# Optimization experiments

Hardware: AMD Instinct MI355X
Metric: run time of the kernel (lower is better)

## Reference

```python
import math
import jax, jax.numpy as jnp
import numpy as np

H = 256      # d_model (number of SSM copies)
N = 32       # half state size (conjugate symmetry)
R = 1        # low-rank correction rank
CH = 1       # channels
L_MAX = 8192 # kernel length (l_max, rate=1.0)


def _r2c(x):
    return x[..., 0] + 1j * x[..., 1]


def _conj(x):
    return jnp.concatenate([x, jnp.conj(x)], axis=-1)


def _mat_power(A, L):
    # A: (H, M, M), L python int; binary exponentiation (powers of A commute)
    out = jnp.broadcast_to(jnp.eye(A.shape[-1], dtype=A.dtype), A.shape)
    while L > 0:
        if L & 1:
            out = jnp.einsum('hij,hjk->hik', out, A)
        A = jnp.einsum('hij,hjk->hik', A, A)
        L >>= 1
    return out


def setup_inputs():
    key = jax.random.key(0)
    ks = jax.random.split(key, 6)
    # log_dt in [log(1e-3), log(1e-1)] as in S4 init
    log_dt = math.log(1e-3) + jax.random.uniform(ks[0], (H,)) * (math.log(1e-1) - math.log(1e-3))
    # inv_w_real = log(-w_real); w_real in (-1.5, -0.5) -> stable discrete system
    inv_w_real = jnp.log(0.5 + jax.random.uniform(ks[1], (H, N)))
    # HiPPO-like imaginary parts: pi * n per state, small jitter
    w_imag = math.pi * jnp.broadcast_to(jnp.arange(N, dtype=jnp.float32), (H, N)) \
             + 0.01 * jax.random.normal(ks[2], (H, N))
    P = 0.5 * jax.random.normal(ks[3], (R, H, N, 2))   # real view of complex (R,H,N)
    B = jax.random.normal(ks[4], (1, H, N, 2))          # real view of complex (1,H,N)
    C = jax.random.normal(ks[5], (CH, H, N, 2))         # real view of complex (CH,H,N)
    return {
        'log_dt': log_dt.astype(jnp.float32),
        'inv_w_real': inv_w_real.astype(jnp.float32),
        'w_imag': w_imag.astype(jnp.float32),
        'P': P.astype(jnp.float32),
        'B': B.astype(jnp.float32),
        'C': C.astype(jnp.float32),
    }


def _kernel(log_dt, inv_w_real, w_imag, P, B, C):
    dt = jnp.exp(log_dt)                              # (H,)  rate = 1.0
    w = -jnp.exp(inv_w_real) + 1j * w_imag            # (H, N) real_type='exp'
    Pc = _r2c(P)                                      # (R, H, N)
    Bc = _r2c(B)                                      # (1, H, N)
    Cc = _r2c(C)                                      # (CH, H, N)
    Qc = jnp.conj(Pc)                                 # (R, H, N)

    # ---- _setup_linear: bilinear-transform discretization pieces ----
    D = 1.0 / (2.0 / dt[:, None] - w)                 # (H, N)
    E = 2.0 / dt[:, None] + w                         # (H, N)
    Rm = jnp.eye(R, dtype=jnp.float32) + 2.0 * jnp.real(
        jnp.einsum('rhn,hn,shn->hrs', Qc, D, Pc))     # (H, R, R)
    QD = jnp.einsum('rhn,hn->hrn', Qc, D)             # (H, R, N)
    Rs = jnp.linalg.solve(Rm.astype(QD.dtype), QD)    # (H, R, N)
    Rs = jnp.transpose(Rs, (1, 0, 2))                 # (R, H, N)

    # ---- _setup_state: dA acting on full 2N-dim (conjugated) state ----
    Dc, Ec, Pc2, Qc2, Rc = (_conj(x) for x in (D, E, Pc, Qc, Rs))
    M = 2 * N
    state = jnp.broadcast_to(jnp.eye(M, dtype=jnp.complex64)[:, None, :], (M, H, M))
    ns = Ec * state - jnp.einsum('rhn,rhm,bhm->bhn', Pc2, Qc2, state)
    ns = Dc * (ns - jnp.einsum('rhn,rhm,bhm->bhn', Pc2, Rc, ns))
    dA = jnp.transpose(ns, (1, 2, 0))                 # (H, M, M)

    # ---- _setup_C: C~ = (I - dA^L)^T C (truncated back to N) ----
    dA_L = _mat_power(dA, L_MAX)                      # (H, M, M)
    C_ = _conj(Cc)                                    # (CH, H, M)
    prod = jnp.einsum('hnm,chn->chm', dA_L, C_)       # contract with dA_L^T
    C_t = (C_ - prod)[..., :N]                        # (CH, H, N)

    # ---- forward: FFT nodes, Cauchy matvec, Woodbury, irfft ----
    Lf = L_MAX // 2 + 1
    omega = jnp.asarray(np.exp(-2j * np.pi / L_MAX), dtype=jnp.complex64) ** jnp.arange(Lf)
    z = 2 * (1 - omega) / (1 + omega)                 # (Lf,)
    w_dt = w * dt[:, None]                            # (H, N)

    Bcat = jnp.concatenate([Bc, Pc], axis=0)          # (1+R, H, N)
    Ccat = jnp.concatenate([C_t, Qc], axis=0)         # (CH+R, H, N)
    v = Bcat[:, None] * Ccat[None]                    # (1+R, CH+R, H, N)
    v = v * dt[None, None, :, None]

    # cauchy_naive with conjugate-pair symmetry
    v_full = _conj(v)                                 # (1+R, CH+R, H, 2N)
    w_full = _conj(w_dt)                              # (H, 2N)
    cauchy = 1.0 / (z[None, None, :] - w_full[..., None])  # (H, 2N, Lf)
    r = jnp.einsum('abhn,hnl->abhl', v_full, cauchy)  # (1+R, CH+R, H, Lf)

    # rank-1 Woodbury correction
    k_f = r[:-1, :-1] - r[:-1, -1:] * r[-1:, :-1] / (1 + r[-1:, -1:])
    k_f = k_f * 2 / (1 + omega)
    k = jnp.fft.irfft(k_f, n=L_MAX, axis=-1)          # (1, CH, H, L)
    return k[-1]                                      # (CH, H, L)


def reference(log_dt, inv_w_real, w_imag, P, B, C):
    return _kernel(log_dt, inv_w_real, w_imag, P, B, C)
```

## Files before the change

### kernel.cpp

```cpp
#include <hip/hip_runtime.h>


#define HH 256
#define NN 32
#define MF 4096

typedef float2 c32;

__device__ __forceinline__ c32 cmul(c32 a, c32 b){ return make_float2(a.x*b.x - a.y*b.y, a.x*b.y + a.y*b.x); }
__device__ __forceinline__ c32 cadd(c32 a, c32 b){ return make_float2(a.x+b.x, a.y+b.y); }
__device__ __forceinline__ c32 csub(c32 a, c32 b){ return make_float2(a.x-b.x, a.y-b.y); }
__device__ __forceinline__ c32 cconjf(c32 a){ return make_float2(a.x, -a.y); }
__device__ __forceinline__ float frcp(float x){ return __builtin_amdgcn_rcpf(x); }

__device__ __forceinline__ float dpp_xor1(float x){
  return __int_as_float(__builtin_amdgcn_update_dpp(0, __float_as_int(x), 0xB1, 0xF, 0xF, true));
}
__device__ __forceinline__ float dpp_xor2(float x){
  return __int_as_float(__builtin_amdgcn_update_dpp(0, __float_as_int(x), 0x4E, 0xF, 0xF, true));
}

__global__ __launch_bounds__(512, 2)
void ssk_S(const float* __restrict__ log_dt, const float* __restrict__ invwr,
           const float* __restrict__ wim, const float* __restrict__ Pin,
           const float* __restrict__ Cin, float* __restrict__ Sws)
{
  __shared__ __align__(16) float4 tA[36];
  __shared__ c32 tB[36];
  __shared__ float red[8*64];
  const int bid = blockIdx.x;
  const int h = bid >> 1;
  const int base = (bid & 1) << 11;
  const int tid = threadIdx.x;

  if (tid < 64) {
    const int n = tid & 31;
    const bool cj = tid >= 32;
    const float dt = expf(log_dt[h]);
    float wr = -expf(invwr[h*NN + n]);
    float wi = wim[h*NN + n];
    if (cj) wi = -wi;
    const float tdt = 2.0f / dt;
    float dr = tdt - wr, di = -wi;
    float invd = 1.0f / (dr*dr + di*di);
    c32 D = make_float2(dr*invd, -di*invd);
    c32 E = make_float2(tdt + wr, wi);
    c32 Pf = make_float2(Pin[(h*NN+n)*2], Pin[(h*NN+n)*2+1]);
    if (cj) Pf.y = -Pf.y;
    c32 Cf = make_float2(Cin[(h*NN+n)*2], Cin[(h*NN+n)*2+1]);
    if (cj) Cf.y = -Cf.y;
    float rm = (Pf.x*Pf.x + Pf.y*Pf.y) * D.x;
    #pragma unroll
    for (int off = 32; off >= 1; off >>= 1) rm += __shfl_xor(rm, off, 64);
    rm += 1.0f;
    c32 Rc = cmul(cconjf(Pf), D);
    float invrm = 1.0f / rm;
    Rc.x *= invrm; Rc.y *= invrm;
    c32 RP = cmul(Rc, Pf);
    #pragma unroll
    for (int off = 32; off >= 1; off >>= 1) {
      RP.x += __shfl_xor(RP.x, off, 64);
      RP.y += __shfl_xor(RP.y, off, 64);
    }
    c32 Q2 = cconjf(Pf);
    c32 s  = csub(cmul(Rc, E), cmul(RP, Q2));
    c32 u  = cadd(Q2, s);
    c32 dd = cmul(D, E);
    c32 pp = cmul(D, Pf);
    c32 pc = cmul(pp, Cf);
    c32 pu = cmul(pp, u);
    if (tid < 32) {
      const int pm = tid + (tid >> 3);
      float ba = 2.0f*(pc.x*dd.x + pc.y*dd.y);
      float bb = 2.0f*(pu.x*dd.x + pu.y*dd.y);
      tA[pm] = make_float4(dd.x, dd.y, pc.x + pc.x, ba);
      tB[pm] = make_float2(pu.x + pu.x, bb);
    }
  }
  __syncthreads();

  const int sub = tid & 3;
  const int grp = tid >> 2;
  const int pbase = sub * 9;

  float pdx[8], pdy[8], paa[8], pba[8], pab[8], pbb[8];
  #pragma unroll
  for (int k = 0; k < 8; k++) {
    float4 A = tA[pbase + k];
    c32 Bv = tB[pbase + k];
    pdx[k] = A.x; pdy[k] = A.y; paa[k] = A.z; pba[k] = A.w;
    pab[k] = Bv.x; pbb[k] = Bv.y;
  }

  float U1x[8], U2x[8];
  #pragma unroll
  for (int k = 0; k < 8; k++) { U1x[k] = 0.0f; U2x[k] = 0.0f; }

  for (int it = 0; it < 16; it++) {
    const int j = base + (it << 7) + grp;
    float rev = (float)j * (1.0f/8192.0f);
    float zx = __builtin_amdgcn_cosf(rev);
    float zy = __builtin_amdgcn_sinf(rev);
    float t2zy = zy + zy;

    float iwxA[8], iwyA[8];
    float Px = 0.0f, Py = 0.0f, Qx = 0.0f, Qy = 0.0f;
    float Rx = 0.0f, Ry = 0.0f, Sx = 0.0f, Sy = 0.0f;
    #pragma unroll
    for (int k = 0; k < 8; k++) {
      float dxx = zx - pdx[k];
      float dy1 = zy - pdy[k];
      float dy2 = zy + pdy[k];
      float xx  = dxx*dxx;
      float p12 = dy1*dy2;
      float wvx = xx - p12;
      float wvyn = dxx*t2zy;
      float den = fmaf(wvx, wvx, wvyn*wvyn);
      float ip  = frcp(den);
      float iwx = wvx*ip;
      float iwy = -wvyn*ip;
      iwxA[k] = iwx; iwyA[k] = iwy;
      Px = fmaf(paa[k], iwx, Px); Py = fmaf(paa[k], iwy, Py);
      Qx = fmaf(pba[k], iwx, Qx); Qy = fmaf(pba[k], iwy, Qy);
      Rx = fmaf(pab[k], iwx, Rx); Ry = fmaf(pab[k], iwy, Ry);
      Sx = fmaf(pbb[k], iwx, Sx); Sy = fmaf(pbb[k], iwy, Sy);
    }
    float ax = fmaf(zx, Px, fmaf(-zy, Py, -Qx));
    float ay = fmaf(zx, Py, fmaf( zy, Px, -Qy));
    float bx = fmaf(zx, Rx, fmaf(-zy, Ry, -Sx));
    float by = fmaf(zx, Ry, fmaf( zy, Rx, -Sy));
    ax += dpp_xor1(ax); ax += dpp_xor2(ax);
    ay += dpp_xor1(ay); ay += dpp_xor2(ay);
    bx += dpp_xor1(bx); bx += dpp_xor2(bx);
    by += dpp_xor1(by); by += dpp_xor2(by);
    float denq = 1.0f + bx, deny = by;
    float idn = frcp(fmaf(denq, denq, deny*deny));
    float tx = (ax*denq + ay*deny)*idn;
    float ty = (ay*denq - ax*deny)*idn;
    float qx = zx*tx - zy*ty;
    float qy = zx*ty + zy*tx;
    if (j == 0) { qx *= 0.5f; qy *= 0.5f; }
    float qzx = qx*zx - qy*zy;
    float qzy = fmaf(qx, zy, qy*zx);
    #pragma unroll
    for (int k = 0; k < 8; k++) {
      float iwx = iwxA[k], iwy = iwyA[k];
      U1x[k] = fmaf(qx,  iwx, fmaf(-qy,  iwy, U1x[k]));
      U2x[k] = fmaf(qzx, iwx, fmaf(-qzy, iwy, U2x[k]));
    }
  }

  float ssx[8], ssy[8];
  #pragma unroll
  for (int k = 0; k < 8; k++) {
    ssx[k] = fmaf(-(pdx[k] + pdx[k]), U1x[k], U2x[k] + U2x[k]);
    ssy[k] = (pdy[k] + pdy[k]) * U1x[k];
  }

  #pragma unroll
  for (int off = 4; off <= 32; off <<= 1) {
    #pragma unroll
    for (int k = 0; k < 8; k++) {
      ssx[k] += __shfl_xor(ssx[k], off, 64);
      ssy[k] += __shfl_xor(ssy[k], off, 64);
    }
  }
  const int lane = tid & 63;
  const int wv = tid >> 6;
  if (lane < 4) {
    #pragma unroll
    for (int k = 0; k < 8; k++) {
      red[wv*64 + lane*16 + 2*k]     = ssx[k];
      red[wv*64 + lane*16 + 2*k + 1] = ssy[k];
    }
  }
  __syncthreads();

  if (tid < 64) {
    float t = 0.0f;
    #pragma unroll
    for (int w = 0; w < 8; w++) t += red[w*64 + tid];
    Sws[bid*64 + tid] = t;
  }
}

__global__ __launch_bounds__(1024, 4)
void ssk_B(const float* __restrict__ log_dt, const float* __restrict__ invwr,
           const float* __restrict__ wim, const float* __restrict__ Pin,
           const float* __restrict__ Bin, const float* __restrict__ Cin,
           const float* __restrict__ Sws, c32* __restrict__ out)
{
  __shared__ __align__(16) c32 Xs[4098];
  __shared__ __align__(16) c32 Zs[4096];
  __shared__ __align__(16) float4 cs1_s[NN];
  __shared__ __align__(16) float4 cs2_s[NN];
  __shared__ c32 cs3_s[NN];
  const int h = blockIdx.x;
  const int tid = threadIdx.x;

  if (tid < 64) {
    const int n = tid & 31;
    const bool cj = tid >= 32;
    const float dt = expf(log_dt[h]);
    float wr = -expf(invwr[h*NN + n]);
    float wi = wim[h*NN + n];
    if (cj) wi = -wi;
    const float tdt = 2.0f / dt;
    float dr = tdt - wr, di = -wi;
    float invd = 1.0f / (dr*dr + di*di);
    c32 D = make_float2(dr*invd, -di*invd);
    c32 E = make_float2(tdt + wr, wi);
    c32 Pf = make_float2(Pin[(h*NN+n)*2], Pin[(h*NN+n)*2+1]);
    if (cj) Pf.y = -Pf.y;
    c32 Cf = make_float2(Cin[(h*NN+n)*2], Cin[(h*NN+n)*2+1]);
    if (cj) Cf.y = -Cf.y;
    float rm = (Pf.x*Pf.x + Pf.y*Pf.y) * D.x;
    #pragma unroll
    for (int off = 32; off >= 1; off >>= 1) rm += __shfl_xor(rm, off, 64);
    rm += 1.0f;
    c32 Rc = cmul(cconjf(Pf), D);
    float invrm = 1.0f / rm;
    Rc.x *= invrm; Rc.y *= invrm;
    c32 RP = cmul(Rc, Pf);
    #pragma unroll
    for (int off = 32; off >= 1; off >>= 1) {
      RP.x += __shfl_xor(RP.x, off, 64);
      RP.y += __shfl_xor(RP.y, off, 64);
    }
    c32 Q2 = cconjf(Pf);
    c32 s  = csub(cmul(Rc, E), cmul(RP, Q2));
    c32 u  = cadd(Q2, s);
    c32 dd = cmul(D, E);
    c32 pp = cmul(D, Pf);
    c32 pc = cmul(pp, Cf);
    c32 pu = cmul(pp, u);

    float dxxn = -1.0f - dd.x;
    float nn1 = fmaf(dxxn, dxxn, dd.y*dd.y);
    float ii = frcp(nn1);
    float glxn = dxxn*ii, glyn = dd.y*ii;
    float aterm = 2.0f*(pc.x*glxn - pc.y*glyn);
    float bterm = 2.0f*(pu.x*glxn - pu.y*glyn);
    #pragma unroll
    for (int off = 16; off >= 1; off >>= 1) {
      aterm += __shfl_xor(aterm, off, 64);
      bterm += __shfl_xor(bterm, off, 64);
    }

    if (tid < 32) {
      const int m = tid;
      c32 dL = dd;
      #pragma unroll
      for (int i2 = 0; i2 < 13; i2++) dL = cmul(dL, dL);
      c32 S;
      S.x = Sws[h*128 + 2*m]     + Sws[h*128 + 64 + 2*m];
      S.y = Sws[h*128 + 2*m + 1] + Sws[h*128 + 64 + 2*m + 1];
      float qn = -aterm * frcp(1.0f + bterm) * 0.5f;
      S.x += qn * 2.0f * glxn;
      S.y += qn * 2.0f * glyn;
      c32 y = cmul(Cf, dL);
      c32 uS = cmul(u, S);
      y.x -= uS.x * (1.0f/8192.0f);
      y.y -= uS.y * (1.0f/8192.0f);
      c32 Ct = csub(Cf, y);
      c32 Bc = make_float2(Bin[(h*NN+m)*2], Bin[(h*NN+m)*2+1]);
      c32 Qc = cconjf(Pf);
      c32 v00 = cmul(Bc, Ct), v01 = cmul(Bc, Qc), v10 = cmul(Pf, Ct), v11 = cmul(Pf, Qc);
      float wx = wr*dt, wy = wi*dt;
      float aw = fmaf(wx, wx, wy*wy);
      float tnw = -(wx + wx);
      float td = dt + dt;
      float a00 = td*v00.x, b00 = td*(v00.x*wx + v00.y*wy);
      float a01 = td*v01.x, b01 = td*(v01.x*wx + v01.y*wy);
      float a10 = td*v10.x, b10 = td*(v10.x*wx + v10.y*wy);
      float a11 = td*v11.x, b11 = td*(v11.x*wx + v11.y*wy);
      cs1_s[m] = make_float4(aw, tnw, a00, b00);
      cs2_s[m] = make_float4(a01, b01, a10, b10);
      cs3_s[m] = make_float2(a11, b11);
      float s00 = v00.x * dt;
      #pragma unroll
      for (int off = 16; off >= 1; off >>= 1) s00 += __shfl_xor(s00, off, 64);
      if (m == 0) Xs[MF] = make_float2(s00, 0.0f);
    }
  }
  __syncthreads();

  {
    float Tq[4], t2[4], t2sq[4];
    c32 a00[4], a01[4], a10[4], a11[4];
    #pragma unroll
    for (int q = 0; q < 4; q++) {
      int j = tid + (q << 10);
      float rev = (float)j * (1.0f/16384.0f);
      float sn = __builtin_amdgcn_sinf(rev);
      float cs = __builtin_amdgcn_cosf(rev);
      float T = sn * frcp(cs);
      Tq[q] = T; t2[q] = 2.0f*T; t2sq[q] = t2[q]*t2[q];
      a00[q] = make_float2(0,0); a01[q] = make_float2(0,0);
      a10[q] = make_float2(0,0); a11[q] = make_float2(0,0);
    }
    #pragma unroll 2
    for (int n = 0; n < NN; n++) {
      float4 C1 = cs1_s[n];
      float4 C2 = cs2_s[n];
      c32   C3 = cs3_s[n];
      #pragma unroll
      for (int q = 0; q < 4; q++) {
        float wvx = C1.x - t2sq[q];
        float wvy = C1.y * t2[q];
        float r = frcp(fmaf(wvx, wvx, wvy*wvy));
        float iwx = wvx*r;
        float iwy = -wvy*r;
        float at;
        at = C1.z*t2[q];
        a00[q].x = fmaf(-C1.w, iwx, fmaf(-at, iwy, a00[q].x));
        a00[q].y = fmaf(-C1.w, iwy, fmaf( at, iwx, a00[q].y));
        at = C2.x*t2[q];
        a01[q].x = fmaf(-C2.y, iwx, fmaf(-at, iwy, a01[q].x));
        a01[q].y = fmaf(-C2.y, iwy, fmaf( at, iwx, a01[q].y));
        at = C2.z*t2[q];
        a10[q].x = fmaf(-C2.w, iwx, fmaf(-at, iwy, a10[q].x));
        a10[q].y = fmaf(-C2.w, iwy, fmaf( at, iwx, a10[q].y));
        at = C3.x*t2[q];
        a11[q].x = fmaf(-C3.y, iwx, fmaf(-at, iwy, a11[q].x));
        a11[q].y = fmaf(-C3.y, iwy, fmaf( at, iwx, a11[q].y));
      }
    }
    #pragma unroll
    for (int q = 0; q < 4; q++) {
      float denx = 1.0f + a11[q].x, deny = a11[q].y;
      float idn = frcp(fmaf(denx, denx, deny*deny));
      c32 invden = make_float2(denx*idn, -deny*idn);
      c32 kf = csub(a00[q], cmul(cmul(a01[q], a10[q]), invden));
      float T = Tq[q];
      Xs[tid + (q << 10)] = make_float2(kf.x - T*kf.y, kf.y + T*kf.x);
    }
  }
  __syncthreads();

  const float invM = 1.0f / (float)MF;
  #pragma unroll
  for (int qq = 0; qq < 4; qq++) {
    int k = tid + (qq << 10);
    c32 Xk = Xs[k];
    c32 Xm = Xs[MF - k];
    float Ex = 0.5f*(Xk.x + Xm.x), Ey = 0.5f*(Xk.y - Xm.y);
    float Ox = 0.5f*(Xk.x - Xm.x), Oy = 0.5f*(Xk.y + Xm.y);
    float rev = (float)k * (1.0f/8192.0f);
    float cs = __builtin_amdgcn_cosf(rev);
    float sn = __builtin_amdgcn_sinf(rev);
    float Orx = Ox*cs - Oy*sn;
    float Ory = Ox*sn + Oy*cs;
    Zs[k] = make_float2((Ex - Ory)*invM, (Ey + Orx)*invM);
  }
  __syncthreads();

  c32* srcf = Zs;
  c32* dstf = Xs;
  int sstride = 1;
  #pragma unroll
  for (int st = 0; st < 6; st++) {
    int jm = tid & ~(sstride - 1);
    float rev = (float)jm * (1.0f/4096.0f);
    float sn = __builtin_amdgcn_sinf(rev);
    float cs = __builtin_amdgcn_cosf(rev);
    c32 w1 = make_float2(cs, sn);
    c32 w2 = cmul(w1, w1);
    c32 w3 = cmul(w2, w1);
    c32 a = srcf[tid];
    c32 b = srcf[tid + 1024];
    c32 c = srcf[tid + 2048];
    c32 d = srcf[tid + 3072];
    c32 apc = cadd(a, c), amc = csub(a, c);
    c32 bpd = cadd(b, d), bmd = csub(b, d);
    int wb = tid + 3*jm;
    dstf[wb] = cadd(apc, bpd);
    dstf[wb + sstride]   = cmul(w1, make_float2(amc.x - bmd.y, amc.y + bmd.x));
    dstf[wb + 2*sstride] = cmul(w2, csub(apc, bpd));
    dstf[wb + 3*sstride] = cmul(w3, make_float2(amc.x + bmd.y, amc.y - bmd.x));
    __syncthreads();
    c32* t = srcf; srcf = dstf; dstf = t;
    sstride <<= 2;
  }

  {
    float4* o4 = (float4*)(out + (size_t)h*MF);
    const float4* s4 = (const float4*)srcf;
    o4[tid] = s4[tid];
    o4[tid + 1024] = s4[tid + 1024];
  }
}

extern "C" void kernel_launch(void* const* d_in, const int* in_sizes, int n_in,
                              void* d_out, int out_size, void* d_ws, size_t ws_size,
                              hipStream_t stream) {
  const float* log_dt = (const float*)d_in[0];
  const float* invwr  = (const float*)d_in[1];
  const float* wimag  = (const float*)d_in[2];
  const float* P      = (const float*)d_in[3];
  const float* B      = (const float*)d_in[4];
  const float* C      = (const float*)d_in[5];
  float* Sws = (float*)d_ws;
  c32*   out = (c32*)d_out;
  (void)in_sizes; (void)n_in; (void)out_size; (void)ws_size;

  ssk_S<<<2*HH, 512, 0, stream>>>(log_dt, invwr, wimag, P, C, Sws);
  ssk_B<<<HH, 1024, 0, stream>>>(log_dt, invwr, wimag, P, B, C, Sws, out);
}
```

Before: 57.36 us.

## Split Cauchy evaluation and FFT into separate kernels with doubled grid

The fused per-head kernel is split into a Cauchy/Woodbury kernel launched over two blocks per head, each handling half of the frequencies, and a separate FFT kernel that reloads the spectrum from global memory. The inner accumulation is rewritten to accumulate separate real and t-scaled terms and combine them once at the end, trimming per-iteration multiplies. The aim is to fill more compute units (512 blocks instead of 256) and cut register pressure for the compute-heavy part. In exchange it adds a kernel launch and a global round trip of the spectrum through the output buffer.

Measured after the change: 60.07 us. 1.05x slower.

```diff
diff --git a/kernel.cpp b/kernel.cpp
--- a/kernel.cpp
+++ b/kernel.cpp
@@ -185,17 +185,18 @@
 }
 
 __global__ __launch_bounds__(1024, 4)
-void ssk_B(const float* __restrict__ log_dt, const float* __restrict__ invwr,
+void ssk_C(const float* __restrict__ log_dt, const float* __restrict__ invwr,
            const float* __restrict__ wim, const float* __restrict__ Pin,
            const float* __restrict__ Bin, const float* __restrict__ Cin,
-           const float* __restrict__ Sws, c32* __restrict__ out)
+           const float* __restrict__ Sws, float* __restrict__ nyq,
+           c32* __restrict__ Xout)
 {
-  __shared__ __align__(16) c32 Xs[4098];
-  __shared__ __align__(16) c32 Zs[4096];
   __shared__ __align__(16) float4 cs1_s[NN];
   __shared__ __align__(16) float4 cs2_s[NN];
   __shared__ c32 cs3_s[NN];
-  const int h = blockIdx.x;
+  const int bid = blockIdx.x;
+  const int h = bid >> 1;
+  const int base = (bid & 1) << 11;
   const int tid = threadIdx.x;
 
   if (tid < 64) {
@@ -280,24 +281,26 @@
       float s00 = v00.x * dt;
       #pragma unroll
       for (int off = 16; off >= 1; off >>= 1) s00 += __shfl_xor(s00, off, 64);
-      if (m == 0) Xs[MF] = make_float2(s00, 0.0f);
+      if (m == 0) nyq[h] = s00;
     }
   }
   __syncthreads();
 
   {
-    float Tq[4], t2[4], t2sq[4];
-    c32 a00[4], a01[4], a10[4], a11[4];
-    #pragma unroll
-    for (int q = 0; q < 4; q++) {
-      int j = tid + (q << 10);
+    float Tq[2], t2[2], t2sq[2];
+    c32 A0[2], B0[2], A1[2], B1[2], A2[2], B2[2], A3[2], B3[2];
+    #pragma unroll
+    for (int q = 0; q < 2; q++) {
+      int j = base + tid + (q << 10);
       float rev = (float)j * (1.0f/16384.0f);
       float sn = __builtin_amdgcn_sinf(rev);
       float cs = __builtin_amdgcn_cosf(rev);
       float T = sn * frcp(cs);
       Tq[q] = T; t2[q] = 2.0f*T; t2sq[q] = t2[q]*t2[q];
-      a00[q] = make_float2(0,0); a01[q] = make_float2(0,0);
-      a10[q] = make_float2(0,0); a11[q] = make_float2(0,0);
+      A0[q] = make_float2(0,0); B0[q] = make_float2(0,0);
+      A1[q] = make_float2(0,0); B1[q] = make_float2(0,0);
+      A2[q] = make_float2(0,0); B2[q] = make_float2(0,0);
+      A3[q] = make_float2(0,0); B3[q] = make_float2(0,0);
     }
     #pragma unroll 2
     for (int n = 0; n < NN; n++) {
@@ -305,36 +308,54 @@
       float4 C2 = cs2_s[n];
       c32   C3 = cs3_s[n];
       #pragma unroll
-      for (int q = 0; q < 4; q++) {
+      for (int q = 0; q < 2; q++) {
         float wvx = C1.x - t2sq[q];
         float wvy = C1.y * t2[q];
         float r = frcp(fmaf(wvx, wvx, wvy*wvy));
         float iwx = wvx*r;
         float iwy = -wvy*r;
-        float at;
-        at = C1.z*t2[q];
-        a00[q].x = fmaf(-C1.w, iwx, fmaf(-at, iwy, a00[q].x));
-        a00[q].y = fmaf(-C1.w, iwy, fmaf( at, iwx, a00[q].y));
-        at = C2.x*t2[q];
-        a01[q].x = fmaf(-C2.y, iwx, fmaf(-at, iwy, a01[q].x));
-        a01[q].y = fmaf(-C2.y, iwy, fmaf( at, iwx, a01[q].y));
-        at = C2.z*t2[q];
-        a10[q].x = fmaf(-C2.w, iwx, fmaf(-at, iwy, a10[q].x));
-        a10[q].y = fmaf(-C2.w, iwy, fmaf( at, iwx, a10[q].y));
-        at = C3.x*t2[q];
-        a11[q].x = fmaf(-C3.y, iwx, fmaf(-at, iwy, a11[q].x));
-        a11[q].y = fmaf(-C3.y, iwy, fmaf( at, iwx, a11[q].y));
+        A0[q].x = fmaf(C1.z, iwx, A0[q].x); A0[q].y = fmaf(C1.z, iwy, A0[q].y);
+        B0[q].x = fmaf(C1.w, iwx, B0[q].x); B0[q].y = fmaf(C1.w, iwy, B0[q].y);
+        A1[q].x = fmaf(C2.x, iwx, A1[q].x); A1[q].y = fmaf(C2.x, iwy, A1[q].y);
+        B1[q].x = fmaf(C2.y, iwx, B1[q].x); B1[q].y = fmaf(C2.y, iwy, B1[q].y);
+        A2[q].x = fmaf(C2.z, iwx, A2[q].x); A2[q].y = fmaf(C2.z, iwy, A2[q].y);
+        B2[q].x = fmaf(C2.w, iwx, B2[q].x); B2[q].y = fmaf(C2.w, iwy, B2[q].y);
+        A3[q].x = fmaf(C3.x, iwx, A3[q].x); A3[q].y = fmaf(C3.x, iwy, A3[q].y);
+        B3[q].x = fmaf(C3.y, iwx, B3[q].x); B3[q].y = fmaf(C3.y, iwy, B3[q].y);
       }
     }
     #pragma unroll
-    for (int q = 0; q < 4; q++) {
-      float denx = 1.0f + a11[q].x, deny = a11[q].y;
+    for (int q = 0; q < 2; q++) {
+      float tt = t2[q];
+      c32 a00 = make_float2(fmaf(-tt, A0[q].y, -B0[q].x), fmaf(tt, A0[q].x, -B0[q].y));
+      c32 a01 = make_float2(fmaf(-tt, A1[q].y, -B1[q].x), fmaf(tt, A1[q].x, -B1[q].y));
+      c32 a10 = make_float2(fmaf(-tt, A2[q].y, -B2[q].x), fmaf(tt, A2[q].x, -B2[q].y));
+      c32 a11 = make_float2(fmaf(-tt, A3[q].y, -B3[q].x), fmaf(tt, A3[q].x, -B3[q].y));
+      float denx = 1.0f + a11.x, deny = a11.y;
       float idn = frcp(fmaf(denx, denx, deny*deny));
       c32 invden = make_float2(denx*idn, -deny*idn);
-      c32 kf = csub(a00[q], cmul(cmul(a01[q], a10[q]), invden));
+      c32 kf = csub(a00, cmul(cmul(a01, a10), invden));
       float T = Tq[q];
-      Xs[tid + (q << 10)] = make_float2(kf.x - T*kf.y, kf.y + T*kf.x);
-    }
+      int j = base + tid + (q << 10);
+      Xout[h*MF + j] = make_float2(kf.x - T*kf.y, kf.y + T*kf.x);
+    }
+  }
+}
+
+__global__ __launch_bounds__(1024, 4)
+void ssk_fft(const float* __restrict__ nyq, c32* __restrict__ io)
+{
+  __shared__ __align__(16) c32 Xs[4098];
+  __shared__ __align__(16) c32 Zs[4096];
+  const int h = blockIdx.x;
+  const int tid = threadIdx.x;
+
+  {
+    float4* Xs4 = (float4*)Xs;
+    const float4* io4 = (const float4*)(io + (size_t)h*MF);
+    Xs4[tid] = io4[tid];
+    Xs4[tid + 1024] = io4[tid + 1024];
+    if (tid == 0) Xs[MF] = make_float2(nyq[h], 0.0f);
   }
   __syncthreads();
 
@@ -384,7 +405,7 @@
   }
 
   {
-    float4* o4 = (float4*)(out + (size_t)h*MF);
+    float4* o4 = (float4*)(io + (size_t)h*MF);
     const float4* s4 = (const float4*)srcf;
     o4[tid] = s4[tid];
     o4[tid + 1024] = s4[tid + 1024];
@@ -401,9 +422,11 @@
   const float* B      = (const float*)d_in[4];
   const float* C      = (const float*)d_in[5];
   float* Sws = (float*)d_ws;
+  float* nyq = (float*)((char*)d_ws + 131072);
   c32*   out = (c32*)d_out;
   (void)in_sizes; (void)n_in; (void)out_size; (void)ws_size;
 
-  ssk_S<<<2*HH, 512, 0, stream>>>(log_dt, invwr, wimag, P, C, Sws);
-  ssk_B<<<HH, 1024, 0, stream>>>(log_dt, invwr, wimag, P, B, C, Sws, out);
-}
+  ssk_S  <<<2*HH, 512,  0, stream>>>(log_dt, invwr, wimag, P, C, Sws);
+  ssk_C  <<<2*HH, 1024, 0, stream>>>(log_dt, invwr, wimag, P, B, C, Sws, nyq, out);
+  ssk_fft<<<HH,   1024, 0, stream>>>(nyq, out);
+}
```
